# Kernel optimization log

Hardware: AMD Instinct MI355X
Metric: run time of the kernel (lower is better)

Reference implementation:

```python
import jax, jax.numpy as jnp
import numpy as np

EPS = 1e-5  # torch LayerNorm default

def _layernorm(x, g, b):
    mu = jnp.mean(x, axis=-1, keepdims=True)
    var = jnp.var(x, axis=-1, keepdims=True)
    return (x - mu) * jax.lax.rsqrt(var + EPS) * g + b

def _mlp(x, g, b, W1, b1, W2, b2):
    # pre-norm LayerNorm -> Linear -> SiLU -> Linear
    h = _layernorm(x, g, b)
    h = jax.nn.silu(h @ W1 + b1)
    return h @ W2 + b2

N, B, F, H = 500_000, 25_000, 128, 64

def setup_inputs() -> dict:
    key = jax.random.key(0)
    ks = jax.random.split(key, 16)
    s = 0.05
    return {
        "pos": jax.random.normal(ks[0], (N, 3), jnp.float32),
        "mass_center": jax.random.normal(ks[1], (B, 3), jnp.float32),
        "scaler": jax.random.normal(ks[2], (N, F), jnp.float32),
        "vector": jax.random.normal(ks[3], (N, 3, F), jnp.float32),
        "batch_index": jnp.sort(jax.random.randint(ks[4], (N,), 0, B)),
        # decoder_alpha params (pre-norm MLP F->H->1)
        "ln_a_g": jnp.ones((F,), jnp.float32),
        "ln_a_b": jnp.zeros((F,), jnp.float32),
        "Wa1": jax.random.normal(ks[5], (F, H), jnp.float32) * s,
        "ba1": jnp.zeros((H,), jnp.float32),
        "Wa2": jax.random.normal(ks[6], (H, 1), jnp.float32) * s,
        "ba2": jnp.zeros((1,), jnp.float32),
        # decoder_nu: gate MLP (pre-norm, F->H->1) + bias-free Linear(F,1)
        "ln_n_g": jnp.ones((F,), jnp.float32),
        "ln_n_b": jnp.zeros((F,), jnp.float32),
        "Wn1": jax.random.normal(ks[7], (F, H), jnp.float32) * s,
        "bn1": jnp.zeros((H,), jnp.float32),
        "Wn2": jax.random.normal(ks[8], (H, 1), jnp.float32) * s,
        "bn2": jnp.zeros((1,), jnp.float32),
        "Wnu": jax.random.normal(ks[9], (F, 1), jnp.float32) * s,
    }

def reference(pos, mass_center, scaler, vector, batch_index,
              ln_a_g, ln_a_b, Wa1, ba1, Wa2, ba2,
              ln_n_g, ln_n_b, Wn1, bn1, Wn2, bn2, Wnu):
    # gather per-node mass center and center positions: [N,3]
    mcv = pos - mass_center[batch_index]
    # Gate: mlp(scaler) [N,1] broadcast-multiplied with vector @ Wnu [N,3,1]
    s_gate = _mlp(scaler, ln_n_g, ln_n_b, Wn1, bn1, Wn2, bn2)       # [N,1]
    v_proj = jnp.einsum('ndf,fo->ndo', vector, Wnu)                  # [N,3,1]
    nu = (s_gate[:, None, :] * v_proj)[..., 0]                       # [N,3]
    # symmetric outer products: [N,3,3]
    outer = nu[:, :, None] * mcv[:, None, :] + mcv[:, :, None] * nu[:, None, :]
    alpha_s = _mlp(scaler, ln_a_g, ln_a_b, Wa1, ba1, Wa2, ba2)       # [N,1]
    alpha = alpha_s[:, :, None] * jnp.eye(3, dtype=alpha_s.dtype) + outer  # [N,3,3]
    # scatter-sum to molecule level, then trace/3
    mol = jax.ops.segment_sum(alpha, batch_index, num_segments=B)    # [B,3,3]
    out = jnp.einsum('bii->b', mol) / 3.0
    return out[:, None]                                              # [B,1]
```

## Files before the change

### kernel.cpp

```cpp
#include <hip/hip_runtime.h>

#define FD 128
#define HD 64
#define NC 128
#define RPB 64

typedef __attribute__((ext_vector_type(8))) short bf16x8;
typedef __attribute__((ext_vector_type(4))) float f32x4;

__device__ __forceinline__ unsigned bfr(float x) {
    unsigned u = __float_as_uint(x);
    return (u + 0x7fffu + ((u >> 16) & 1u)) >> 16;
}

__global__ void prep_kernel(
    const float* __restrict__ lnag, const float* __restrict__ lnab,
    const float* __restrict__ Wa1, const float* __restrict__ ba1, const float* __restrict__ Wa2,
    const float* __restrict__ lnng, const float* __restrict__ lnnb,
    const float* __restrict__ Wn1, const float* __restrict__ bn1, const float* __restrict__ Wn2,
    unsigned short* __restrict__ wq, float* __restrict__ c, float* __restrict__ w2)
{
    int n = threadIdx.x;
    const float* W  = (n < HD) ? Wa1 : Wn1;
    const float* g  = (n < HD) ? lnag : lnng;
    const float* bb = (n < HD) ? lnab : lnnb;
    const float* b1 = (n < HD) ? ba1 : bn1;
    const float* W2 = (n < HD) ? Wa2 : Wn2;
    int h = n & (HD - 1);
    float accb = b1[h];
    for (int f = 0; f < FD; ++f) {
        float w = W[f * HD + h];
        wq[n * FD + f] = (unsigned short)bfr(g[f] * w);
        accb += bb[f] * w;
    }
    c[n] = accb;
    w2[n] = W2[h];
}

__global__ __launch_bounds__(256, 4) void fused_kernel(
    const float* __restrict__ scaler, const float* __restrict__ vec,
    const float* __restrict__ wnu, const float* __restrict__ pos,
    const float* __restrict__ mc, const int* __restrict__ bidx,
    const unsigned short* __restrict__ wq, const float* __restrict__ c,
    const float* __restrict__ w2, const float* __restrict__ ba2,
    const float* __restrict__ bn2, float* __restrict__ out, int n_nodes)
{
    __shared__ float tl[4][16];

    int tid = threadIdx.x;
    int lane = tid & 63, w = tid >> 6;
    int rowbase = blockIdx.x * RPB + w * 16;
    int lrow = lane & 15, lgrp = lane >> 4;

    int xnode = rowbase + lrow;
    int gx = xnode < n_nodes ? xnode : (n_nodes - 1);
    const float4* xp = reinterpret_cast<const float4*>(scaler + (size_t)gx * FD);
    float4 xv[8];
#pragma unroll
    for (int ks = 0; ks < 4; ++ks) {
        xv[2 * ks]     = xp[ks * 8 + lgrp * 2];
        xv[2 * ks + 1] = xp[ks * 8 + lgrp * 2 + 1];
    }

    {
        int o = lane >> 3, cc = lane & 7;
        float4 wn4[4];
#pragma unroll
        for (int m = 0; m < 4; ++m)
            wn4[m] = reinterpret_cast<const float4*>(wnu)[m * 8 + cc];
#pragma unroll
        for (int g = 0; g < 2; ++g) {
            int row = g * 8 + o;
            int node = rowbase + row;
            int n = node < n_nodes ? node : (n_nodes - 1);
            int b = bidx[n];
            float m0 = pos[n * 3 + 0] - mc[b * 3 + 0];
            float m1 = pos[n * 3 + 1] - mc[b * 3 + 1];
            float m2 = pos[n * 3 + 2] - mc[b * 3 + 2];
            const float4* vr = reinterpret_cast<const float4*>(vec + (size_t)n * 3 * FD);
            float acc = 0.f;
#pragma unroll
            for (int k = 0; k < 12; ++k) {
                float4 v = vr[cc + k * 8];
                float4 wnv = wn4[k & 3];
                float d4 = v.x * wnv.x + v.y * wnv.y + v.z * wnv.z + v.w * wnv.w;
                float mm = (k < 4) ? m0 : (k < 8 ? m1 : m2);
                acc = fmaf(d4, mm, acc);
            }
            acc += __shfl_xor(acc, 1);
            acc += __shfl_xor(acc, 2);
            acc += __shfl_xor(acc, 4);
            if (cc == 0) tl[w][row] = acc;
        }
    }

    float s = 0.f, s2 = 0.f;
#pragma unroll
    for (int i = 0; i < 8; ++i) {
        float4 v = xv[i];
        s  += v.x + v.y + v.z + v.w;
        s2 += v.x * v.x + v.y * v.y + v.z * v.z + v.w * v.w;
    }
    s  += __shfl_xor(s, 16);  s  += __shfl_xor(s, 32);
    s2 += __shfl_xor(s2, 16); s2 += __shfl_xor(s2, 32);
    float mu = s * (1.f / FD);
    float var = s2 * (1.f / FD) - mu * mu;
    float rstd = rsqrtf(var + 1e-5f);

    bf16x8 af[4];
#pragma unroll
    for (int ks = 0; ks < 4; ++ks) {
        float4 a = xv[2 * ks], b = xv[2 * ks + 1];
        union { unsigned u[4]; bf16x8 v; } pk;
        pk.u[0] = bfr((a.x - mu) * rstd) | (bfr((a.y - mu) * rstd) << 16);
        pk.u[1] = bfr((a.z - mu) * rstd) | (bfr((a.w - mu) * rstd) << 16);
        pk.u[2] = bfr((b.x - mu) * rstd) | (bfr((b.y - mu) * rstd) << 16);
        pk.u[3] = bfr((b.z - mu) * rstd) | (bfr((b.w - mu) * rstd) << 16);
        af[ks] = pk.v;
    }

    float pa[4] = {0.f, 0.f, 0.f, 0.f}, pn[4] = {0.f, 0.f, 0.f, 0.f};
#pragma unroll
    for (int tile = 0; tile < 8; ++tile) {
        f32x4 acc = {0.f, 0.f, 0.f, 0.f};
        int n = tile * 16 + lrow;
        const bf16x8* brow = reinterpret_cast<const bf16x8*>(wq + n * FD);
#pragma unroll
        for (int ks = 0; ks < 4; ++ks) {
            bf16x8 bf = brow[ks * 4 + lgrp];
            acc = __builtin_amdgcn_mfma_f32_16x16x32_bf16(af[ks], bf, acc, 0, 0, 0);
        }
        int col = tile * 16 + lrow;
        float bias = c[col], w2v = w2[col];
#pragma unroll
        for (int r = 0; r < 4; ++r) {
            float h1 = acc[r] + bias;
            float y = h1 / (1.f + __expf(-h1));
            float cb = y * w2v;
            if (tile < 4) pa[r] += cb; else pn[r] += cb;
        }
    }
#pragma unroll
    for (int off = 1; off < 16; off <<= 1) {
#pragma unroll
        for (int r = 0; r < 4; ++r) {
            pa[r] += __shfl_xor(pa[r], off);
            pn[r] += __shfl_xor(pn[r], off);
        }
    }
    if (lrow == 0) {
        float b2a = ba2[0], b2n = bn2[0];
#pragma unroll
        for (int r = 0; r < 4; ++r) {
            int nl = lgrp * 4 + r;
            int node = rowbase + nl;
            if (node < n_nodes) {
                float val = (pa[r] + b2a) + (2.f / 3.f) * (pn[r] + b2n) * tl[w][nl];
                atomicAdd(out + bidx[node], val);
            }
        }
    }
}

extern "C" void kernel_launch(void* const* d_in, const int* in_sizes, int n_in,
                              void* d_out, int out_size, void* d_ws, size_t ws_size,
                              hipStream_t stream) {
    const float* pos    = (const float*)d_in[0];
    const float* mc     = (const float*)d_in[1];
    const float* scaler = (const float*)d_in[2];
    const float* vec    = (const float*)d_in[3];
    const int*   bidx   = (const int*)d_in[4];
    const float* lnag   = (const float*)d_in[5];
    const float* lnab   = (const float*)d_in[6];
    const float* Wa1    = (const float*)d_in[7];
    const float* ba1    = (const float*)d_in[8];
    const float* Wa2    = (const float*)d_in[9];
    const float* ba2    = (const float*)d_in[10];
    const float* lnng   = (const float*)d_in[11];
    const float* lnnb   = (const float*)d_in[12];
    const float* Wn1    = (const float*)d_in[13];
    const float* bn1    = (const float*)d_in[14];
    const float* Wn2    = (const float*)d_in[15];
    const float* bn2    = (const float*)d_in[16];
    const float* Wnu    = (const float*)d_in[17];

    int N = in_sizes[0] / 3;
    int B = in_sizes[1] / 3;

    unsigned short* wq = (unsigned short*)d_ws;
    float* c  = (float*)((char*)d_ws + NC * FD * 2);
    float* w2 = c + NC;

    hipMemsetAsync(d_out, 0, (size_t)B * sizeof(float), stream);

    hipLaunchKernelGGL(prep_kernel, dim3(1), dim3(NC), 0, stream,
                       lnag, lnab, Wa1, ba1, Wa2, lnng, lnnb, Wn1, bn1, Wn2, wq, c, w2);

    int blocks = (N + RPB - 1) / RPB;
    hipLaunchKernelGGL(fused_kernel, dim3(blocks), dim3(256), 0, stream,
                       scaler, vec, Wnu, pos, mc, bidx, wq, c, w2, ba2, bn2,
                       (float*)d_out, N);
}
```

Baseline: 251.3 us.

## Split fused kernel into separate vector-projection and MLP kernels

Moves the vector·Wnu·mcv projection out of the fused MLP kernel into its own streaming kernel. That kernel uses half a wave per node and writes a per-node scalar to workspace, which the MLP kernel then reads. The aim is better occupancy and memory streaming for the large vector read, free of the MFMA kernel's register pressure. The cost is an extra launch and a global round trip for the N-length intermediate.

```diff
diff --git a/kernel.cpp b/kernel.cpp
--- a/kernel.cpp
+++ b/kernel.cpp
@@ -3,7 +3,6 @@
 #define FD 128
 #define HD 64
 #define NC 128
-#define RPB 64
 
 typedef __attribute__((ext_vector_type(8))) short bf16x8;
 typedef __attribute__((ext_vector_type(4))) float f32x4;
@@ -37,19 +36,43 @@
     w2[n] = W2[h];
 }
 
-__global__ __launch_bounds__(256, 4) void fused_kernel(
-    const float* __restrict__ scaler, const float* __restrict__ vec,
-    const float* __restrict__ wnu, const float* __restrict__ pos,
-    const float* __restrict__ mc, const int* __restrict__ bidx,
+__global__ __launch_bounds__(256, 8) void vec_kernel(
+    const float* __restrict__ vec, const float* __restrict__ wnu,
+    const float* __restrict__ pos, const float* __restrict__ mc,
+    const int* __restrict__ bidx, float* __restrict__ t, int n_nodes)
+{
+    int gid = (int)(blockIdx.x * blockDim.x + threadIdx.x);
+    int wave = gid >> 6;
+    int lane = threadIdx.x & 63;
+    int h = lane >> 5, j = lane & 31;
+    int node = wave * 2 + h;
+    bool valid = node < n_nodes;
+    int n = valid ? node : (n_nodes - 1);
+    const float4* vr = reinterpret_cast<const float4*>(vec + (size_t)n * 3 * FD);
+    float4 v0 = vr[j], v1 = vr[32 + j], v2 = vr[64 + j];
+    float4 wn = reinterpret_cast<const float4*>(wnu)[j];
+    int b = bidx[n];
+    float m0 = pos[n * 3 + 0] - mc[b * 3 + 0];
+    float m1 = pos[n * 3 + 1] - mc[b * 3 + 1];
+    float m2 = pos[n * 3 + 2] - mc[b * 3 + 2];
+    float acc = (v0.x * wn.x + v0.y * wn.y + v0.z * wn.z + v0.w * wn.w) * m0
+              + (v1.x * wn.x + v1.y * wn.y + v1.z * wn.z + v1.w * wn.w) * m1
+              + (v2.x * wn.x + v2.y * wn.y + v2.z * wn.z + v2.w * wn.w) * m2;
+#pragma unroll
+    for (int off = 16; off; off >>= 1) acc += __shfl_xor(acc, off);
+    if (j == 0 && valid) t[node] = acc;
+}
+
+__global__ __launch_bounds__(256, 4) void mlp_kernel(
+    const float* __restrict__ scaler, const float* __restrict__ t,
+    const int* __restrict__ bidx,
     const unsigned short* __restrict__ wq, const float* __restrict__ c,
     const float* __restrict__ w2, const float* __restrict__ ba2,
     const float* __restrict__ bn2, float* __restrict__ out, int n_nodes)
 {
-    __shared__ float tl[4][16];
-
     int tid = threadIdx.x;
     int lane = tid & 63, w = tid >> 6;
-    int rowbase = blockIdx.x * RPB + w * 16;
+    int rowbase = blockIdx.x * 64 + w * 16;
     int lrow = lane & 15, lgrp = lane >> 4;
 
     int xnode = rowbase + lrow;
@@ -60,38 +83,6 @@
     for (int ks = 0; ks < 4; ++ks) {
         xv[2 * ks]     = xp[ks * 8 + lgrp * 2];
         xv[2 * ks + 1] = xp[ks * 8 + lgrp * 2 + 1];
-    }
-
-    {
-        int o = lane >> 3, cc = lane & 7;
-        float4 wn4[4];
-#pragma unroll
-        for (int m = 0; m < 4; ++m)
-            wn4[m] = reinterpret_cast<const float4*>(wnu)[m * 8 + cc];
-#pragma unroll
-        for (int g = 0; g < 2; ++g) {
-            int row = g * 8 + o;
-            int node = rowbase + row;
-            int n = node < n_nodes ? node : (n_nodes - 1);
-            int b = bidx[n];
-            float m0 = pos[n * 3 + 0] - mc[b * 3 + 0];
-            float m1 = pos[n * 3 + 1] - mc[b * 3 + 1];
-            float m2 = pos[n * 3 + 2] - mc[b * 3 + 2];
-            const float4* vr = reinterpret_cast<const float4*>(vec + (size_t)n * 3 * FD);
-            float acc = 0.f;
-#pragma unroll
-            for (int k = 0; k < 12; ++k) {
-                float4 v = vr[cc + k * 8];
-                float4 wnv = wn4[k & 3];
-                float d4 = v.x * wnv.x + v.y * wnv.y + v.z * wnv.z + v.w * wnv.w;
-                float mm = (k < 4) ? m0 : (k < 8 ? m1 : m2);
-                acc = fmaf(d4, mm, acc);
-            }
-            acc += __shfl_xor(acc, 1);
-            acc += __shfl_xor(acc, 2);
-            acc += __shfl_xor(acc, 4);
-            if (cc == 0) tl[w][row] = acc;
-        }
     }
 
     float s = 0.f, s2 = 0.f;
@@ -152,10 +143,9 @@
         float b2a = ba2[0], b2n = bn2[0];
 #pragma unroll
         for (int r = 0; r < 4; ++r) {
-            int nl = lgrp * 4 + r;
-            int node = rowbase + nl;
+            int node = rowbase + lgrp * 4 + r;
             if (node < n_nodes) {
-                float val = (pa[r] + b2a) + (2.f / 3.f) * (pn[r] + b2n) * tl[w][nl];
+                float val = (pa[r] + b2a) + (2.f / 3.f) * (pn[r] + b2n) * t[node];
                 atomicAdd(out + bidx[node], val);
             }
         }
@@ -190,14 +180,18 @@
     unsigned short* wq = (unsigned short*)d_ws;
     float* c  = (float*)((char*)d_ws + NC * FD * 2);
     float* w2 = c + NC;
+    float* t  = w2 + NC;
 
     hipMemsetAsync(d_out, 0, (size_t)B * sizeof(float), stream);
 
     hipLaunchKernelGGL(prep_kernel, dim3(1), dim3(NC), 0, stream,
                        lnag, lnab, Wa1, ba1, Wa2, lnng, lnnb, Wn1, bn1, Wn2, wq, c, w2);
 
-    int blocks = (N + RPB - 1) / RPB;
-    hipLaunchKernelGGL(fused_kernel, dim3(blocks), dim3(256), 0, stream,
-                       scaler, vec, Wnu, pos, mc, bidx, wq, c, w2, ba2, bn2,
-                       (float*)d_out, N);
+    int vblocks = (N + 7) / 8;
+    hipLaunchKernelGGL(vec_kernel, dim3(vblocks), dim3(256), 0, stream,
+                       vec, Wnu, pos, mc, bidx, t, N);
+
+    int mblocks = (N + 63) / 64;
+    hipLaunchKernelGGL(mlp_kernel, dim3(mblocks), dim3(256), 0, stream,
+                       scaler, t, bidx, wq, c, w2, ba2, bn2, (float*)d_out, N);
 }
```

Result: slower. 305.0 us (+21.3%).

## Convert fused kernel to persistent grid-stride loop over 16-row wave tiles

Applied to the files above, without the earlier changes.

Launches a fixed grid of up to 1024 blocks and has each wave loop over 16-node tiles in grid-stride order, instead of one block per 64 nodes. Per-wave constants (the Wnu slice and the output biases) are now loaded once before the loop rather than once per tile. The aim is to cut block launch and setup overhead on a memory-bound workload. The cost is that there is no cross-iteration prefetch, so memory latency hiding depends on resident waves alone, and the fixed grid may leave the tail unevenly balanced.

```diff
diff --git a/kernel.cpp b/kernel.cpp
--- a/kernel.cpp
+++ b/kernel.cpp
@@ -3,7 +3,6 @@
 #define FD 128
 #define HD 64
 #define NC 128
-#define RPB 64
 
 typedef __attribute__((ext_vector_type(8))) short bf16x8;
 typedef __attribute__((ext_vector_type(4))) float f32x4;
@@ -43,31 +42,37 @@
     const float* __restrict__ mc, const int* __restrict__ bidx,
     const unsigned short* __restrict__ wq, const float* __restrict__ c,
     const float* __restrict__ w2, const float* __restrict__ ba2,
-    const float* __restrict__ bn2, float* __restrict__ out, int n_nodes)
+    const float* __restrict__ bn2, float* __restrict__ out,
+    int n_nodes, int ntiles)
 {
     __shared__ float tl[4][16];
 
     int tid = threadIdx.x;
     int lane = tid & 63, w = tid >> 6;
-    int rowbase = blockIdx.x * RPB + w * 16;
     int lrow = lane & 15, lgrp = lane >> 4;
-
-    int xnode = rowbase + lrow;
-    int gx = xnode < n_nodes ? xnode : (n_nodes - 1);
-    const float4* xp = reinterpret_cast<const float4*>(scaler + (size_t)gx * FD);
-    float4 xv[8];
-#pragma unroll
-    for (int ks = 0; ks < 4; ++ks) {
-        xv[2 * ks]     = xp[ks * 8 + lgrp * 2];
-        xv[2 * ks + 1] = xp[ks * 8 + lgrp * 2 + 1];
-    }
-
-    {
-        int o = lane >> 3, cc = lane & 7;
-        float4 wn4[4];
-#pragma unroll
-        for (int m = 0; m < 4; ++m)
-            wn4[m] = reinterpret_cast<const float4*>(wnu)[m * 8 + cc];
+    int gwave = blockIdx.x * 4 + w;
+    int nwaves = gridDim.x * 4;
+
+    int o = lane >> 3, cc = lane & 7;
+    float4 wn4[4];
+#pragma unroll
+    for (int m = 0; m < 4; ++m)
+        wn4[m] = reinterpret_cast<const float4*>(wnu)[m * 8 + cc];
+    float b2a = ba2[0], b2n = bn2[0];
+
+    for (int tile_i = gwave; tile_i < ntiles; tile_i += nwaves) {
+        int rowbase = tile_i * 16;
+
+        int xnode = rowbase + lrow;
+        int gx = xnode < n_nodes ? xnode : (n_nodes - 1);
+        const float4* xp = reinterpret_cast<const float4*>(scaler + (size_t)gx * FD);
+        float4 xv[8];
+#pragma unroll
+        for (int ks = 0; ks < 4; ++ks) {
+            xv[2 * ks]     = xp[ks * 8 + lgrp * 2];
+            xv[2 * ks + 1] = xp[ks * 8 + lgrp * 2 + 1];
+        }
+
 #pragma unroll
         for (int g = 0; g < 2; ++g) {
             int row = g * 8 + o;
@@ -92,71 +97,69 @@
             acc += __shfl_xor(acc, 4);
             if (cc == 0) tl[w][row] = acc;
         }
-    }
-
-    float s = 0.f, s2 = 0.f;
-#pragma unroll
-    for (int i = 0; i < 8; ++i) {
-        float4 v = xv[i];
-        s  += v.x + v.y + v.z + v.w;
-        s2 += v.x * v.x + v.y * v.y + v.z * v.z + v.w * v.w;
-    }
-    s  += __shfl_xor(s, 16);  s  += __shfl_xor(s, 32);
-    s2 += __shfl_xor(s2, 16); s2 += __shfl_xor(s2, 32);
-    float mu = s * (1.f / FD);
-    float var = s2 * (1.f / FD) - mu * mu;
-    float rstd = rsqrtf(var + 1e-5f);
-
-    bf16x8 af[4];
-#pragma unroll
-    for (int ks = 0; ks < 4; ++ks) {
-        float4 a = xv[2 * ks], b = xv[2 * ks + 1];
-        union { unsigned u[4]; bf16x8 v; } pk;
-        pk.u[0] = bfr((a.x - mu) * rstd) | (bfr((a.y - mu) * rstd) << 16);
-        pk.u[1] = bfr((a.z - mu) * rstd) | (bfr((a.w - mu) * rstd) << 16);
-        pk.u[2] = bfr((b.x - mu) * rstd) | (bfr((b.y - mu) * rstd) << 16);
-        pk.u[3] = bfr((b.z - mu) * rstd) | (bfr((b.w - mu) * rstd) << 16);
-        af[ks] = pk.v;
-    }
-
-    float pa[4] = {0.f, 0.f, 0.f, 0.f}, pn[4] = {0.f, 0.f, 0.f, 0.f};
-#pragma unroll
-    for (int tile = 0; tile < 8; ++tile) {
-        f32x4 acc = {0.f, 0.f, 0.f, 0.f};
-        int n = tile * 16 + lrow;
-        const bf16x8* brow = reinterpret_cast<const bf16x8*>(wq + n * FD);
+
+        float s = 0.f, s2 = 0.f;
+#pragma unroll
+        for (int i = 0; i < 8; ++i) {
+            float4 v = xv[i];
+            s  += v.x + v.y + v.z + v.w;
+            s2 += v.x * v.x + v.y * v.y + v.z * v.z + v.w * v.w;
+        }
+        s  += __shfl_xor(s, 16);  s  += __shfl_xor(s, 32);
+        s2 += __shfl_xor(s2, 16); s2 += __shfl_xor(s2, 32);
+        float mu = s * (1.f / FD);
+        float var = s2 * (1.f / FD) - mu * mu;
+        float rstd = rsqrtf(var + 1e-5f);
+
+        bf16x8 af[4];
 #pragma unroll
         for (int ks = 0; ks < 4; ++ks) {
-            bf16x8 bf = brow[ks * 4 + lgrp];
-            acc = __builtin_amdgcn_mfma_f32_16x16x32_bf16(af[ks], bf, acc, 0, 0, 0);
-        }
-        int col = tile * 16 + lrow;
-        float bias = c[col], w2v = w2[col];
-#pragma unroll
-        for (int r = 0; r < 4; ++r) {
-            float h1 = acc[r] + bias;
-            float y = h1 / (1.f + __expf(-h1));
-            float cb = y * w2v;
-            if (tile < 4) pa[r] += cb; else pn[r] += cb;
-        }
-    }
-#pragma unroll
-    for (int off = 1; off < 16; off <<= 1) {
-#pragma unroll
-        for (int r = 0; r < 4; ++r) {
-            pa[r] += __shfl_xor(pa[r], off);
-            pn[r] += __shfl_xor(pn[r], off);
-        }
-    }
-    if (lrow == 0) {
-        float b2a = ba2[0], b2n = bn2[0];
-#pragma unroll
-        for (int r = 0; r < 4; ++r) {
-            int nl = lgrp * 4 + r;
-            int node = rowbase + nl;
-            if (node < n_nodes) {
-                float val = (pa[r] + b2a) + (2.f / 3.f) * (pn[r] + b2n) * tl[w][nl];
-                atomicAdd(out + bidx[node], val);
+            float4 a = xv[2 * ks], b = xv[2 * ks + 1];
+            union { unsigned u[4]; bf16x8 v; } pk;
+            pk.u[0] = bfr((a.x - mu) * rstd) | (bfr((a.y - mu) * rstd) << 16);
+            pk.u[1] = bfr((a.z - mu) * rstd) | (bfr((a.w - mu) * rstd) << 16);
+            pk.u[2] = bfr((b.x - mu) * rstd) | (bfr((b.y - mu) * rstd) << 16);
+            pk.u[3] = bfr((b.z - mu) * rstd) | (bfr((b.w - mu) * rstd) << 16);
+            af[ks] = pk.v;
+        }
+
+        float pa[4] = {0.f, 0.f, 0.f, 0.f}, pn[4] = {0.f, 0.f, 0.f, 0.f};
+#pragma unroll
+        for (int tc = 0; tc < 8; ++tc) {
+            f32x4 acc = {0.f, 0.f, 0.f, 0.f};
+            int n = tc * 16 + lrow;
+            const bf16x8* brow = reinterpret_cast<const bf16x8*>(wq + n * FD);
+#pragma unroll
+            for (int ks = 0; ks < 4; ++ks) {
+                bf16x8 bf = brow[ks * 4 + lgrp];
+                acc = __builtin_amdgcn_mfma_f32_16x16x32_bf16(af[ks], bf, acc, 0, 0, 0);
+            }
+            int col = tc * 16 + lrow;
+            float bias = c[col], w2v = w2[col];
+#pragma unroll
+            for (int r = 0; r < 4; ++r) {
+                float h1 = acc[r] + bias;
+                float y = h1 / (1.f + __expf(-h1));
+                float cb = y * w2v;
+                if (tc < 4) pa[r] += cb; else pn[r] += cb;
+            }
+        }
+#pragma unroll
+        for (int off = 1; off < 16; off <<= 1) {
+#pragma unroll
+            for (int r = 0; r < 4; ++r) {
+                pa[r] += __shfl_xor(pa[r], off);
+                pn[r] += __shfl_xor(pn[r], off);
+            }
+        }
+        if (lrow == 0) {
+#pragma unroll
+            for (int r = 0; r < 4; ++r) {
+                int node = rowbase + lgrp * 4 + r;
+                if (node < n_nodes) {
+                    float val = (pa[r] + b2a) + (2.f / 3.f) * (pn[r] + b2n) * tl[w][lgrp * 4 + r];
+                    atomicAdd(out + bidx[node], val);
+                }
             }
         }
     }
@@ -196,8 +199,10 @@
     hipLaunchKernelGGL(prep_kernel, dim3(1), dim3(NC), 0, stream,
                        lnag, lnab, Wa1, ba1, Wa2, lnng, lnnb, Wn1, bn1, Wn2, wq, c, w2);
 
-    int blocks = (N + RPB - 1) / RPB;
-    hipLaunchKernelGGL(fused_kernel, dim3(blocks), dim3(256), 0, stream,
+    int ntiles = (N + 15) / 16;
+    int nblocks = 1024;
+    if (nblocks * 4 > ntiles) nblocks = (ntiles + 3) / 4;
+    hipLaunchKernelGGL(fused_kernel, dim3(nblocks), dim3(256), 0, stream,
                        scaler, vec, Wnu, pos, mc, bidx, wq, c, w2, ba2, bn2,
-                       (float*)d_out, N);
-}
+                       (float*)d_out, N, ntiles);
+}
```

After: 393.0 us. +56.3%, slower.

## Replace per-node atomic scatter with per-node buffer plus segmented reduce kernel

Applied to the files above, without the earlier changes.

The fused kernel now writes each node's scalar contribution to a workspace buffer with vectorized stores instead of issuing an atomicAdd per node into the output. A new reduce kernel gives each molecule one thread, which binary-searches the sorted batch index for its segment and sums it, so the output memset is no longer needed. This removes atomic contention and makes the summation order deterministic. The cost is an extra kernel launch, a 2 MB buffer written and read back, and binary searches over the index array.

```diff
diff --git a/kernel.cpp b/kernel.cpp
--- a/kernel.cpp
+++ b/kernel.cpp
@@ -43,7 +43,7 @@
     const float* __restrict__ mc, const int* __restrict__ bidx,
     const unsigned short* __restrict__ wq, const float* __restrict__ c,
     const float* __restrict__ w2, const float* __restrict__ ba2,
-    const float* __restrict__ bn2, float* __restrict__ out, int n_nodes)
+    const float* __restrict__ bn2, float* __restrict__ val, int n_nodes)
 {
     __shared__ float tl[4][16];
 
@@ -150,16 +150,37 @@
     }
     if (lrow == 0) {
         float b2a = ba2[0], b2n = bn2[0];
+        float tmp[4];
 #pragma unroll
         for (int r = 0; r < 4; ++r) {
             int nl = lgrp * 4 + r;
-            int node = rowbase + nl;
-            if (node < n_nodes) {
-                float val = (pa[r] + b2a) + (2.f / 3.f) * (pn[r] + b2n) * tl[w][nl];
-                atomicAdd(out + bidx[node], val);
-            }
-        }
-    }
+            tmp[r] = (pa[r] + b2a) + (2.f / 3.f) * (pn[r] + b2n) * tl[w][nl];
+        }
+        int node0 = rowbase + lgrp * 4;
+        if (node0 + 3 < n_nodes) {
+            *reinterpret_cast<float4*>(val + node0) = make_float4(tmp[0], tmp[1], tmp[2], tmp[3]);
+        } else {
+#pragma unroll
+            for (int r = 0; r < 4; ++r)
+                if (node0 + r < n_nodes) val[node0 + r] = tmp[r];
+        }
+    }
+}
+
+__global__ __launch_bounds__(256) void reduce_kernel(
+    const float* __restrict__ val, const int* __restrict__ bidx,
+    float* __restrict__ out, int n_nodes, int n_batch)
+{
+    int b = (int)(blockIdx.x * blockDim.x + threadIdx.x);
+    if (b >= n_batch) return;
+    int lo = 0, hi = n_nodes;
+    while (lo < hi) { int mid = (lo + hi) >> 1; if (bidx[mid] < b) lo = mid + 1; else hi = mid; }
+    int s0 = lo;
+    hi = n_nodes;
+    while (lo < hi) { int mid = (lo + hi) >> 1; if (bidx[mid] <= b) lo = mid + 1; else hi = mid; }
+    float acc = 0.f;
+    for (int i = s0; i < lo; ++i) acc += val[i];
+    out[b] = acc;
 }
 
 extern "C" void kernel_launch(void* const* d_in, const int* in_sizes, int n_in,
@@ -190,8 +211,7 @@
     unsigned short* wq = (unsigned short*)d_ws;
     float* c  = (float*)((char*)d_ws + NC * FD * 2);
     float* w2 = c + NC;
-
-    hipMemsetAsync(d_out, 0, (size_t)B * sizeof(float), stream);
+    float* val = w2 + NC;
 
     hipLaunchKernelGGL(prep_kernel, dim3(1), dim3(NC), 0, stream,
                        lnag, lnab, Wa1, ba1, Wa2, lnng, lnnb, Wn1, bn1, Wn2, wq, c, w2);
@@ -199,5 +219,9 @@
     int blocks = (N + RPB - 1) / RPB;
     hipLaunchKernelGGL(fused_kernel, dim3(blocks), dim3(256), 0, stream,
                        scaler, vec, Wnu, pos, mc, bidx, wq, c, w2, ba2, bn2,
-                       (float*)d_out, N);
-}
+                       val, N);
+
+    int rblocks = (B + 255) / 256;
+    hipLaunchKernelGGL(reduce_kernel, dim3(rblocks), dim3(256), 0, stream,
+                       val, bidx, (float*)d_out, N, B);
+}
```

Measured after the change: 245.5 us. 2.3% less time.
